# Performance work log

Measured on AMD Instinct MI355X. Metric: run time of the kernel, lower is better.

Reference implementation:

```python
import jax, jax.numpy as jnp
import numpy as np

B, S, D = 32, 512, 512      # batch, seq, feature
E, H, O, K = 8, 2048, 512, 2  # experts, expert hidden, expert out, top_k


def setup_inputs() -> dict:
    key = jax.random.key(0)
    ks = jax.random.split(key, 5)
    sc = lambda k, shape, scale: jax.random.normal(k, shape, jnp.float32) * scale
    return {
        "x": sc(ks[0], (B, S, D), 1.0),
        "attn_w": sc(ks[1], (D, 1), 0.05),
        "attn_b": jnp.zeros((1,), jnp.float32),
        "gate_w": sc(ks[2], (D, E), 0.05),
        "gate_b": jnp.zeros((E,), jnp.float32),
        "w1": sc(ks[3], (E, D, H), 0.02),
        "b1": jnp.zeros((E, H), jnp.float32),
        "w2": sc(ks[4], (E, H, O), 0.02),
        "b2": jnp.zeros((E, O), jnp.float32),
    }


def reference(x, attn_w, attn_b, gate_w, gate_b, w1, b1, w2, b2):
    # --- attention pooling over the sequence axis ---
    scores = x @ attn_w + attn_b                      # [B,S,1]
    aw = jax.nn.softmax(scores, axis=1)               # softmax over seq
    pooled = jnp.sum(x * aw, axis=1)                  # [B,D]

    # --- gating: softmax -> top-k mask -> renormalize ---
    gates = jax.nn.softmax(pooled @ gate_w + gate_b, axis=-1)  # [B,E]
    _, idx = jax.lax.top_k(gates, K)                  # [B,K]
    mask = jnp.sum(jax.nn.one_hot(idx, E, dtype=gates.dtype), axis=-2)  # [B,E]
    g = gates * mask
    g = g / (jnp.sum(g, axis=-1, keepdims=True) + 1e-9)        # [B,E]

    # --- dense all-experts compute (exact GELU, as keras Dense('gelu')) ---
    h = jax.nn.gelu(jnp.einsum('bsd,edh->ebsh', x, w1) + b1[:, None, None, :],
                    approximate=False)                 # [E,B,S,H]
    eo = jax.nn.gelu(jnp.einsum('ebsh,eho->ebso', h, w2) + b2[:, None, None, :],
                     approximate=False)                # [E,B,S,O]

    # --- weighted combine over experts ---
    return jnp.einsum('ebso,be->bso', eo, g)           # [B,S,O]
```

## Files before the change

kernel.cpp:

```cpp
#include <hip/hip_runtime.h>
#include <hip/hip_bf16.h>
#include <math.h>

#define B_  32
#define S_  512
#define D_  512
#define E_  8
#define H_  2048
#define O_  512

typedef __bf16 bf16x8 __attribute__((ext_vector_type(8)));
typedef float  f32x4  __attribute__((ext_vector_type(4)));

#define GL2LDS(src, dst) \
  __builtin_amdgcn_global_load_lds((const __attribute__((address_space(1))) void*)(src), \
                                   (__attribute__((address_space(3))) void*)(dst), 16, 0, 0)

__device__ __forceinline__ float gelu_fast(float v) {
  float w = v * fmaf(v * v, 0.0713548162f, 1.5957691216f);
  float e = __expf(-w);
  return v * __builtin_amdgcn_rcpf(1.0f + e);
}

__device__ __forceinline__ float gelu_exact(float v) {
  return 0.5f * v * (1.0f + erff(v * 0.70710678118654752f));
}

__global__ __launch_bounds__(256) void pool_gate_kernel(
    const float* __restrict__ x, const float* __restrict__ attn_w,
    const float* __restrict__ attn_b, const float* __restrict__ gate_w,
    const float* __restrict__ gate_b, int* __restrict__ gidx, float* __restrict__ gwt)
{
  __shared__ float sc[512];
  __shared__ float pooled[512];
  __shared__ float red[8];
  const int tid = threadIdx.x;
  const int b = blockIdx.x;
  const float* xb = x + (size_t)b * S_ * D_;
  const float ab = attn_b[0];

  for (int s = tid; s < S_; s += 256) {
    const float4* xr = (const float4*)(xb + (size_t)s * D_);
    const float4* wr = (const float4*)attn_w;
    float acc = 0.f;
    for (int i = 0; i < D_ / 4; ++i) {
      float4 xv = xr[i], wv = wr[i];
      acc += xv.x * wv.x + xv.y * wv.y + xv.z * wv.z + xv.w * wv.w;
    }
    sc[s] = acc + ab;
  }
  __syncthreads();

  float m = fmaxf(sc[tid], sc[tid + 256]);
  for (int off = 32; off; off >>= 1) m = fmaxf(m, __shfl_down(m, off));
  if ((tid & 63) == 0) red[tid >> 6] = m;
  __syncthreads();
  if (tid == 0) red[0] = fmaxf(fmaxf(red[0], red[1]), fmaxf(red[2], red[3]));
  __syncthreads();
  m = red[0];
  float e0 = expf(sc[tid] - m), e1 = expf(sc[tid + 256] - m);
  float ssum = e0 + e1;
  for (int off = 32; off; off >>= 1) ssum += __shfl_down(ssum, off);
  if ((tid & 63) == 0) red[4 + (tid >> 6)] = ssum;
  __syncthreads();
  if (tid == 0) red[4] = red[4] + red[5] + red[6] + red[7];
  __syncthreads();
  float inv = 1.f / red[4];
  sc[tid] = e0 * inv;
  sc[tid + 256] = e1 * inv;
  __syncthreads();

  float p0 = 0.f, p1 = 0.f;
  for (int s = 0; s < S_; ++s) {
    float awv = sc[s];
    p0 += awv * xb[(size_t)s * D_ + tid];
    p1 += awv * xb[(size_t)s * D_ + tid + 256];
  }
  pooled[tid] = p0;
  pooled[tid + 256] = p1;
  __syncthreads();

  if (tid < E_) {
    float z = gate_b[tid];
    for (int d = 0; d < D_; ++d) z += pooled[d] * gate_w[d * E_ + tid];
    red[tid] = z;
  }
  __syncthreads();
  if (tid == 0) {
    float zmax = red[0];
    for (int i = 1; i < E_; ++i) zmax = fmaxf(zmax, red[i]);
    float ge[E_]; float zs = 0.f;
    for (int i = 0; i < E_; ++i) { ge[i] = expf(red[i] - zmax); zs += ge[i]; }
    for (int i = 0; i < E_; ++i) ge[i] /= zs;
    int i0 = 0;
    for (int i = 1; i < E_; ++i) if (ge[i] > ge[i0]) i0 = i;
    int i1 = -1;
    for (int i = 0; i < E_; ++i) if (i != i0 && (i1 < 0 || ge[i] > ge[i1])) i1 = i;
    float denom = ge[i0] + ge[i1] + 1e-9f;
    gidx[b * 2 + 0] = i0; gidx[b * 2 + 1] = i1;
    gwt[b * 2 + 0] = ge[i0] / denom; gwt[b * 2 + 1] = ge[i1] / denom;
  }
}

__global__ void psort_kernel(const int* __restrict__ gidx, int* __restrict__ psort) {
  if (threadIdx.x == 0 && blockIdx.x == 0) {
    int cnt[E_];
    for (int e = 0; e < E_; ++e) cnt[e] = 0;
    for (int p = 0; p < 2 * B_; ++p) cnt[gidx[p]]++;
    int pos[E_]; int s = 0;
    for (int e = 0; e < E_; ++e) { pos[e] = s; s += cnt[e]; }
    for (int p = 0; p < 2 * B_; ++p) psort[pos[gidx[p]]++] = p;
  }
}

__global__ void cast_x_kernel(const float* __restrict__ in, ushort* __restrict__ outp, int n) {
  int i = blockIdx.x * blockDim.x + threadIdx.x;
  const int n4 = n >> 2;
  for (; i < n4; i += gridDim.x * blockDim.x) {
    float4 v = ((const float4*)in)[i];
    ushort4 o;
    o.x = __builtin_bit_cast(unsigned short, __float2bfloat16(v.x));
    o.y = __builtin_bit_cast(unsigned short, __float2bfloat16(v.y));
    o.z = __builtin_bit_cast(unsigned short, __float2bfloat16(v.z));
    o.w = __builtin_bit_cast(unsigned short, __float2bfloat16(v.w));
    ((ushort4*)outp)[i] = o;
  }
}

__global__ void transpose_cast_kernel(const float* __restrict__ in,
                                      __hip_bfloat16* __restrict__ outT, int R, int C)
{
  __shared__ float tile[32][33];
  const int z = blockIdx.z;
  const float* inz = in + (size_t)z * R * C;
  __hip_bfloat16* outz = outT + (size_t)z * R * C;
  const int c0 = blockIdx.x * 32, r0 = blockIdx.y * 32;
  const int tx = threadIdx.x, ty = threadIdx.y;
#pragma unroll
  for (int jj = 0; jj < 4; ++jj) {
    int r = r0 + ty + jj * 8;
    tile[ty + jj * 8][tx] = inz[(size_t)r * C + c0 + tx];
  }
  __syncthreads();
#pragma unroll
  for (int jj = 0; jj < 4; ++jj) {
    int c = c0 + ty + jj * 8;
    outz[(size_t)c * R + r0 + tx] = __float2bfloat16(tile[tx][ty + jj * 8]);
  }
}

__device__ __forceinline__ void gemm_core(const char* __restrict__ Wg, const char* __restrict__ Xg,
                                          const int ldw, const int ldx, const int NT,
                                          char* lds, f32x4 (&acc)[4][4])
{
  const int tid = threadIdx.x;
  const int l = tid & 63;
  const int w = tid >> 6;
  const int wh = w >> 1;
  const int ws = w & 1;
  const int lr = l & 15;
  const int kc16 = ((l >> 4) & 3) << 4;
  const int swz = (lr & 7) << 4;
  const int kA = kc16 ^ swz;
  const int kB = (64 + kc16) ^ swz;
  const int aoff = wh * 8192 + lr * 128;
  const int boff = 32768 + ws * 8192 + lr * 128;

  const int rw = tid >> 3;
  const int cs = ((tid & 7) << 4) ^ ((rw & 7) << 4);
  const int dst = tid * 16;
  const char* pW0 = Wg + (size_t)(rw      ) * ldw + cs;
  const char* pW1 = Wg + (size_t)(rw +  64) * ldw + cs;
  const char* pW2 = Wg + (size_t)(rw + 128) * ldw + cs;
  const char* pW3 = Wg + (size_t)(rw + 192) * ldw + cs;
  const char* pX0 = Xg + (size_t)(rw      ) * ldx + cs;
  const char* pX1 = Xg + (size_t)(rw +  64) * ldx + cs;

  {
    char* q0 = lds;
    GL2LDS(pW0, q0 + dst);          GL2LDS(pW1, q0 + 8192 + dst);
    GL2LDS(pW2, q0 + 16384 + dst);  GL2LDS(pW3, q0 + 24576 + dst);
    GL2LDS(pX0, q0 + 32768 + dst);  GL2LDS(pX1, q0 + 40960 + dst);
    char* q1 = lds + 49152;
    GL2LDS(pW0 + 128, q1 + dst);          GL2LDS(pW1 + 128, q1 + 8192 + dst);
    GL2LDS(pW2 + 128, q1 + 16384 + dst);  GL2LDS(pW3 + 128, q1 + 24576 + dst);
    GL2LDS(pX0 + 128, q1 + 32768 + dst);  GL2LDS(pX1 + 128, q1 + 40960 + dst);
    pW0 += 256; pW1 += 256; pW2 += 256; pW3 += 256; pX0 += 256; pX1 += 256;
  }

  for (int t = 0; t < NT; ++t) {
    char* cur = lds + (t % 3) * 49152;
    char* nb  = lds + ((t + 2) % 3) * 49152;
    const bool pre = (t + 2 < NT);

    if (pre) {
      GL2LDS(pW0, nb + dst);
      GL2LDS(pW1, nb + 8192 + dst);
      GL2LDS(pW2, nb + 16384 + dst);
    }
    if (pre)             asm volatile("s_waitcnt vmcnt(9)" ::: "memory");
    else if (t + 1 < NT) asm volatile("s_waitcnt vmcnt(6)" ::: "memory");
    else                 asm volatile("s_waitcnt vmcnt(0)" ::: "memory");
    __builtin_amdgcn_s_barrier();
    __builtin_amdgcn_sched_barrier(0);
    {
      bf16x8 af[4], bfv[4];
#pragma unroll
      for (int r = 0; r < 4; ++r) af[r]  = *(const bf16x8*)(cur + aoff + r * 2048 + kA);
#pragma unroll
      for (int n = 0; n < 4; ++n) bfv[n] = *(const bf16x8*)(cur + boff + n * 2048 + kA);
      __builtin_amdgcn_s_setprio(1);
#pragma unroll
      for (int r = 0; r < 4; ++r)
#pragma unroll
        for (int n = 0; n < 4; ++n)
          acc[r][n] = __builtin_amdgcn_mfma_f32_16x16x32_bf16(af[r], bfv[n], acc[r][n], 0, 0, 0);
      __builtin_amdgcn_s_setprio(0);
    }
    __builtin_amdgcn_sched_barrier(0);
    __builtin_amdgcn_s_barrier();

    if (pre) {
      GL2LDS(pW3, nb + 24576 + dst);
      GL2LDS(pX0, nb + 32768 + dst);
      GL2LDS(pX1, nb + 40960 + dst);
      pW0 += 128; pW1 += 128; pW2 += 128; pW3 += 128; pX0 += 128; pX1 += 128;
    }
    {
      bf16x8 af[4], bfv[4];
#pragma unroll
      for (int r = 0; r < 4; ++r) af[r]  = *(const bf16x8*)(cur + aoff + r * 2048 + kB);
#pragma unroll
      for (int n = 0; n < 4; ++n) bfv[n] = *(const bf16x8*)(cur + boff + n * 2048 + kB);
      __builtin_amdgcn_s_setprio(1);
#pragma unroll
      for (int r = 0; r < 4; ++r)
#pragma unroll
        for (int n = 0; n < 4; ++n)
          acc[r][n] = __builtin_amdgcn_mfma_f32_16x16x32_bf16(af[r], bfv[n], acc[r][n], 0, 0, 0);
      __builtin_amdgcn_s_setprio(0);
    }
    __builtin_amdgcn_sched_barrier(0);
    __builtin_amdgcn_s_barrier();
  }
}

__global__ __launch_bounds__(512, 2) void gemm1_kernel(
    const __hip_bfloat16* __restrict__ Xb, const __hip_bfloat16* __restrict__ W1T,
    const float* __restrict__ b1, __hip_bfloat16* __restrict__ Hbuf,
    const int* __restrict__ gidx, const int* __restrict__ psort)
{
  extern __shared__ char lds[];
  const int nblk = gridDim.x * gridDim.y;
  const int P = blockIdx.y * gridDim.x + blockIdx.x;
  const int L = (P & 7) * (nblk >> 3) + (P >> 3);
  const int pairL = L >> 5;
  const int tl = L & 31;
  const int p = psort[pairL];
  const int b = p >> 1;
  const int e = gidx[p];
  const int s0 = (tl >> 3) * 128;
  const int h0 = (tl & 7) * 256;
  const char* Wg = (const char*)(W1T + ((size_t)e * H_ + h0) * D_);
  const char* Xg = (const char*)(Xb + ((size_t)b * S_ + s0) * D_);
  f32x4 acc[4][4] = {};
  gemm_core(Wg, Xg, D_ * 2, D_ * 2, D_ / 64, lds, acc);

  const int tid = threadIdx.x, l = tid & 63, w = tid >> 6;
  const int wh = w >> 1, ws = w & 1, lr = l & 15, hi4 = ((l >> 4) & 3) << 2;
  const float* b1e = b1 + (size_t)e * H_ + h0;
  __hip_bfloat16* Hp = Hbuf + (size_t)p * S_ * H_;
#pragma unroll
  for (int r = 0; r < 4; ++r) {
    const int hl = wh * 64 + r * 16 + hi4;
    const float4 bias = *(const float4*)(b1e + hl);
#pragma unroll
    for (int n = 0; n < 4; ++n) {
      const int sl = s0 + ws * 64 + n * 16 + lr;
      ushort4 ov;
      ov.x = __builtin_bit_cast(unsigned short, __float2bfloat16(gelu_fast(acc[r][n][0] + bias.x)));
      ov.y = __builtin_bit_cast(unsigned short, __float2bfloat16(gelu_fast(acc[r][n][1] + bias.y)));
      ov.z = __builtin_bit_cast(unsigned short, __float2bfloat16(gelu_fast(acc[r][n][2] + bias.z)));
      ov.w = __builtin_bit_cast(unsigned short, __float2bfloat16(gelu_fast(acc[r][n][3] + bias.w)));
      *(ushort4*)(Hp + (size_t)sl * H_ + h0 + hl) = ov;
    }
  }
}

__global__ __launch_bounds__(512, 2) void gemm2_kernel(
    const __hip_bfloat16* __restrict__ Hbuf, const __hip_bfloat16* __restrict__ W2T,
    const float* __restrict__ b2, float* __restrict__ out,
    const int* __restrict__ gidx, const float* __restrict__ gwt)
{
  extern __shared__ char lds[];
  const int nblk = gridDim.x * gridDim.y;
  const int P = blockIdx.y * gridDim.x + blockIdx.x;
  const int L = (P & 7) * (nblk >> 3) + (P >> 3);
  const int b = L >> 3;
  const int tl = L & 7;
  const int s0 = (tl >> 1) * 128;
  const int o0 = (tl & 1) * 256;

  const int tid = threadIdx.x, l = tid & 63, w = tid >> 6;
  const int wh = w >> 1, ws = w & 1, lr = l & 15, hi4 = ((l >> 4) & 3) << 2;

  f32x4 fout[4][4] = {};
  for (int slot = 0; slot < 2; ++slot) {
    const int p = b * 2 + slot;
    const int e = gidx[p];
    const float gw = gwt[p];
    const char* Wg = (const char*)(W2T + ((size_t)e * O_ + o0) * H_);
    const char* Xg = (const char*)(Hbuf + ((size_t)p * S_ + s0) * H_);
    f32x4 acc[4][4] = {};
    gemm_core(Wg, Xg, H_ * 2, H_ * 2, H_ / 64, lds, acc);
    const float* b2e = b2 + (size_t)e * O_ + o0;
#pragma unroll
    for (int r = 0; r < 4; ++r) {
      const int ol = wh * 64 + r * 16 + hi4;
      const float4 bias = *(const float4*)(b2e + ol);
#pragma unroll
      for (int n = 0; n < 4; ++n) {
        fout[r][n][0] += gelu_fast(acc[r][n][0] + bias.x) * gw;
        fout[r][n][1] += gelu_fast(acc[r][n][1] + bias.y) * gw;
        fout[r][n][2] += gelu_fast(acc[r][n][2] + bias.z) * gw;
        fout[r][n][3] += gelu_fast(acc[r][n][3] + bias.w) * gw;
      }
    }
  }

#pragma unroll
  for (int r = 0; r < 4; ++r) {
    const int ol = wh * 64 + r * 16 + hi4;
#pragma unroll
    for (int n = 0; n < 4; ++n) {
      const int sl = s0 + ws * 64 + n * 16 + lr;
      *(float4*)(out + ((size_t)b * S_ + sl) * O_ + o0 + ol) =
          (float4){fout[r][n][0], fout[r][n][1], fout[r][n][2], fout[r][n][3]};
    }
  }
}

__global__ void sentinel_kernel(float* out, int n) {
  int i = blockIdx.x * blockDim.x + threadIdx.x;
  for (; i < n; i += gridDim.x * blockDim.x) out[i] = 1.0e6f;
}

extern "C" void kernel_launch(void* const* d_in, const int* in_sizes, int n_in,
                              void* d_out, int out_size, void* d_ws, size_t ws_size,
                              hipStream_t stream)
{
  const float* x      = (const float*)d_in[0];
  const float* attn_w = (const float*)d_in[1];
  const float* attn_b = (const float*)d_in[2];
  const float* gate_w = (const float*)d_in[3];
  const float* gate_b = (const float*)d_in[4];
  const float* w1     = (const float*)d_in[5];
  const float* b1     = (const float*)d_in[6];
  const float* w2     = (const float*)d_in[7];
  const float* b2     = (const float*)d_in[8];
  float* out = (float*)d_out;

  char* ws = (char*)d_ws;
  const size_t OFF_GIDX = 0;
  const size_t OFF_GWT  = 256;
  const size_t OFF_PSRT = 512;
  const size_t OFF_X    = 1024;
  const size_t SZ_X     = (size_t)B_ * S_ * D_ * 2;
  const size_t OFF_W1T  = OFF_X + SZ_X;
  const size_t SZ_W1T   = (size_t)E_ * H_ * D_ * 2;
  const size_t OFF_W2T  = OFF_W1T + SZ_W1T;
  const size_t SZ_W2T   = (size_t)E_ * O_ * H_ * 2;
  const size_t OFF_H    = OFF_W2T + SZ_W2T;
  const size_t PAIR_H   = (size_t)S_ * H_ * 2;

  if (OFF_H + 64 * PAIR_H > ws_size) {
    hipLaunchKernelGGL(sentinel_kernel, dim3(256), dim3(256), 0, stream, out, out_size);
    return;
  }

  int*   gidx  = (int*)(ws + OFF_GIDX);
  float* gwt   = (float*)(ws + OFF_GWT);
  int*   psort = (int*)(ws + OFF_PSRT);
  __hip_bfloat16* xb   = (__hip_bfloat16*)(ws + OFF_X);
  __hip_bfloat16* w1T  = (__hip_bfloat16*)(ws + OFF_W1T);
  __hip_bfloat16* w2T  = (__hip_bfloat16*)(ws + OFF_W2T);
  __hip_bfloat16* Hbuf = (__hip_bfloat16*)(ws + OFF_H);

  (void)hipFuncSetAttribute((const void*)gemm1_kernel, hipFuncAttributeMaxDynamicSharedMemorySize, 147456);
  (void)hipFuncSetAttribute((const void*)gemm2_kernel, hipFuncAttributeMaxDynamicSharedMemorySize, 147456);

  hipLaunchKernelGGL(pool_gate_kernel, dim3(B_), dim3(256), 0, stream,
                     x, attn_w, attn_b, gate_w, gate_b, gidx, gwt);
  hipLaunchKernelGGL(psort_kernel, dim3(1), dim3(64), 0, stream, gidx, psort);
  hipLaunchKernelGGL(cast_x_kernel, dim3(2048), dim3(256), 0, stream,
                     x, (ushort*)xb, B_ * S_ * D_);
  hipLaunchKernelGGL(transpose_cast_kernel, dim3(H_ / 32, D_ / 32, E_), dim3(32, 8), 0, stream,
                     w1, w1T, D_, H_);
  hipLaunchKernelGGL(transpose_cast_kernel, dim3(O_ / 32, H_ / 32, E_), dim3(32, 8), 0, stream,
                     w2, w2T, H_, O_);

  hipLaunchKernelGGL(gemm1_kernel, dim3(32, 64), dim3(512), 147456, stream,
                     xb, w1T, b1, Hbuf, gidx, psort);
  hipLaunchKernelGGL(gemm2_kernel, dim3(8, 32), dim3(512), 147456, stream,
                     Hbuf, w2T, b2, out, gidx, gwt);
}
```

Measured before the change: 290.0 us.

## Parallelize attention pooling and run persistent continuous-K pipelines in both expert GEMMs

The single 32-block pool/gate kernel is split into four stages: a fused bf16 cast plus score dot-product, a per-batch softmax, a pooling kernel spread over a 4x32 grid, and a combined gate/top-k/sort kernel. The attention bias is dropped because softmax over the sequence is shift-invariant. GEMM1 now launches 256 blocks, and each block streams all 8 H tiles through one continuous triple-buffered pipeline, writing its epilogue every 8 steps. GEMM2 chains both expert slots into a single 64-step pipeline, which removes the pipeline drain and refill between slots. The cost is fewer blocks per GPU, which lowers occupancy and load balancing, and the score, weight and pooled scratch buffers now live in the H buffer region.

After: 269.3 us. 7.2% less time.

```diff
diff --git a/kernel.cpp b/kernel.cpp
--- a/kernel.cpp
+++ b/kernel.cpp
@@ -22,108 +22,123 @@
   return v * __builtin_amdgcn_rcpf(1.0f + e);
 }
 
-__device__ __forceinline__ float gelu_exact(float v) {
-  return 0.5f * v * (1.0f + erff(v * 0.70710678118654752f));
-}
-
-__global__ __launch_bounds__(256) void pool_gate_kernel(
+__global__ __launch_bounds__(256) void cast_score_kernel(
     const float* __restrict__ x, const float* __restrict__ attn_w,
-    const float* __restrict__ attn_b, const float* __restrict__ gate_w,
-    const float* __restrict__ gate_b, int* __restrict__ gidx, float* __restrict__ gwt)
-{
-  __shared__ float sc[512];
-  __shared__ float pooled[512];
-  __shared__ float red[8];
-  const int tid = threadIdx.x;
-  const int b = blockIdx.x;
-  const float* xb = x + (size_t)b * S_ * D_;
-  const float ab = attn_b[0];
-
-  for (int s = tid; s < S_; s += 256) {
-    const float4* xr = (const float4*)(xb + (size_t)s * D_);
-    const float4* wr = (const float4*)attn_w;
-    float acc = 0.f;
-    for (int i = 0; i < D_ / 4; ++i) {
-      float4 xv = xr[i], wv = wr[i];
-      acc += xv.x * wv.x + xv.y * wv.y + xv.z * wv.z + xv.w * wv.w;
-    }
-    sc[s] = acc + ab;
-  }
-  __syncthreads();
-
-  float m = fmaxf(sc[tid], sc[tid + 256]);
-  for (int off = 32; off; off >>= 1) m = fmaxf(m, __shfl_down(m, off));
-  if ((tid & 63) == 0) red[tid >> 6] = m;
-  __syncthreads();
-  if (tid == 0) red[0] = fmaxf(fmaxf(red[0], red[1]), fmaxf(red[2], red[3]));
-  __syncthreads();
-  m = red[0];
-  float e0 = expf(sc[tid] - m), e1 = expf(sc[tid + 256] - m);
-  float ssum = e0 + e1;
-  for (int off = 32; off; off >>= 1) ssum += __shfl_down(ssum, off);
-  if ((tid & 63) == 0) red[4 + (tid >> 6)] = ssum;
-  __syncthreads();
-  if (tid == 0) red[4] = red[4] + red[5] + red[6] + red[7];
-  __syncthreads();
-  float inv = 1.f / red[4];
-  sc[tid] = e0 * inv;
-  sc[tid + 256] = e1 * inv;
-  __syncthreads();
-
-  float p0 = 0.f, p1 = 0.f;
-  for (int s = 0; s < S_; ++s) {
-    float awv = sc[s];
-    p0 += awv * xb[(size_t)s * D_ + tid];
-    p1 += awv * xb[(size_t)s * D_ + tid + 256];
-  }
-  pooled[tid] = p0;
-  pooled[tid + 256] = p1;
-  __syncthreads();
-
-  if (tid < E_) {
-    float z = gate_b[tid];
-    for (int d = 0; d < D_; ++d) z += pooled[d] * gate_w[d * E_ + tid];
-    red[tid] = z;
-  }
-  __syncthreads();
-  if (tid == 0) {
-    float zmax = red[0];
-    for (int i = 1; i < E_; ++i) zmax = fmaxf(zmax, red[i]);
-    float ge[E_]; float zs = 0.f;
-    for (int i = 0; i < E_; ++i) { ge[i] = expf(red[i] - zmax); zs += ge[i]; }
-    for (int i = 0; i < E_; ++i) ge[i] /= zs;
-    int i0 = 0;
-    for (int i = 1; i < E_; ++i) if (ge[i] > ge[i0]) i0 = i;
-    int i1 = -1;
-    for (int i = 0; i < E_; ++i) if (i != i0 && (i1 < 0 || ge[i] > ge[i1])) i1 = i;
-    float denom = ge[i0] + ge[i1] + 1e-9f;
-    gidx[b * 2 + 0] = i0; gidx[b * 2 + 1] = i1;
-    gwt[b * 2 + 0] = ge[i0] / denom; gwt[b * 2 + 1] = ge[i1] / denom;
-  }
-}
-
-__global__ void psort_kernel(const int* __restrict__ gidx, int* __restrict__ psort) {
-  if (threadIdx.x == 0 && blockIdx.x == 0) {
-    int cnt[E_];
-    for (int e = 0; e < E_; ++e) cnt[e] = 0;
-    for (int p = 0; p < 2 * B_; ++p) cnt[gidx[p]]++;
-    int pos[E_]; int s = 0;
-    for (int e = 0; e < E_; ++e) { pos[e] = s; s += cnt[e]; }
-    for (int p = 0; p < 2 * B_; ++p) psort[pos[gidx[p]]++] = p;
-  }
-}
-
-__global__ void cast_x_kernel(const float* __restrict__ in, ushort* __restrict__ outp, int n) {
-  int i = blockIdx.x * blockDim.x + threadIdx.x;
-  const int n4 = n >> 2;
-  for (; i < n4; i += gridDim.x * blockDim.x) {
-    float4 v = ((const float4*)in)[i];
+    ushort* __restrict__ xb, float* __restrict__ scores)
+{
+  const int t = threadIdx.x;
+  const int r = t >> 5;
+  const int cg = t & 31;
+  const int row = blockIdx.x * 8 + r;
+  const float* src  = x + (size_t)row * D_ + cg * 16;
+  const float* wsrc = attn_w + cg * 16;
+  ushort* dstp = xb + (size_t)row * D_ + cg * 16;
+  float acc = 0.f;
+#pragma unroll
+  for (int k = 0; k < 4; ++k) {
+    float4 v  = *(const float4*)(src + k * 4);
+    float4 wv = *(const float4*)(wsrc + k * 4);
+    acc += v.x * wv.x + v.y * wv.y + v.z * wv.z + v.w * wv.w;
     ushort4 o;
     o.x = __builtin_bit_cast(unsigned short, __float2bfloat16(v.x));
     o.y = __builtin_bit_cast(unsigned short, __float2bfloat16(v.y));
     o.z = __builtin_bit_cast(unsigned short, __float2bfloat16(v.z));
     o.w = __builtin_bit_cast(unsigned short, __float2bfloat16(v.w));
-    ((ushort4*)outp)[i] = o;
+    *(ushort4*)(dstp + k * 4) = o;
+  }
+#pragma unroll
+  for (int off = 16; off; off >>= 1) acc += __shfl_xor(acc, off);
+  if (cg == 0) scores[row] = acc;
+}
+
+__global__ __launch_bounds__(512) void softmax_aw_kernel(
+    const float* __restrict__ scores, float* __restrict__ aw)
+{
+  __shared__ float red[8];
+  __shared__ float mm, ss;
+  const int t = threadIdx.x, b = blockIdx.x;
+  float v = scores[b * S_ + t];
+  float m = v;
+#pragma unroll
+  for (int off = 32; off; off >>= 1) m = fmaxf(m, __shfl_xor(m, off));
+  if ((t & 63) == 0) red[t >> 6] = m;
+  __syncthreads();
+  if (t == 0) {
+    float a = red[0];
+    for (int i = 1; i < 8; ++i) a = fmaxf(a, red[i]);
+    mm = a;
+  }
+  __syncthreads();
+  float e = expf(v - mm);
+  float s = e;
+#pragma unroll
+  for (int off = 32; off; off >>= 1) s += __shfl_xor(s, off);
+  if ((t & 63) == 0) red[t >> 6] = s;
+  __syncthreads();
+  if (t == 0) {
+    float a = 0.f;
+    for (int i = 0; i < 8; ++i) a += red[i];
+    ss = 1.f / a;
+  }
+  __syncthreads();
+  aw[b * S_ + t] = e * ss;
+}
+
+__global__ __launch_bounds__(512) void pool_kernel(
+    const float* __restrict__ x, const float* __restrict__ aw, float* __restrict__ pooled)
+{
+  __shared__ float sm[4][128];
+  const int t = threadIdx.x;
+  const int dl = t & 127;
+  const int sh = t >> 7;
+  const int b = blockIdx.y;
+  const int d = blockIdx.x * 128 + dl;
+  const float* xp  = x + (size_t)b * S_ * D_ + d;
+  const float* awb = aw + b * S_;
+  float acc = 0.f;
+#pragma unroll 4
+  for (int s = sh; s < S_; s += 4)
+    acc = fmaf(awb[s], xp[(size_t)s * D_], acc);
+  if (sh) sm[sh][dl] = acc;
+  __syncthreads();
+  if (sh == 0) pooled[b * D_ + d] = acc + sm[1][dl] + sm[2][dl] + sm[3][dl];
+}
+
+__global__ __launch_bounds__(256) void gate_psort_kernel(
+    const float* __restrict__ pooled, const float* __restrict__ gate_w,
+    const float* __restrict__ gate_b, int* __restrict__ gidx, float* __restrict__ gwt,
+    int* __restrict__ psort)
+{
+  __shared__ float gl[32][8];
+  const int t = threadIdx.x;
+  const int b = t >> 3, ee = t & 7;
+  float z = gate_b[ee];
+  const float* pb = pooled + b * D_;
+  for (int d = 0; d < D_; ++d) z = fmaf(pb[d], gate_w[d * E_ + ee], z);
+  gl[b][ee] = z;
+  __syncthreads();
+  if (t < 32) {
+    float ge[8];
+    float zmax = gl[t][0];
+    for (int i = 1; i < 8; ++i) zmax = fmaxf(zmax, gl[t][i]);
+    float zs = 0.f;
+    for (int i = 0; i < 8; ++i) { ge[i] = expf(gl[t][i] - zmax); zs += ge[i]; }
+    for (int i = 0; i < 8; ++i) ge[i] /= zs;
+    int i0 = 0;
+    for (int i = 1; i < 8; ++i) if (ge[i] > ge[i0]) i0 = i;
+    int i1 = -1;
+    for (int i = 0; i < 8; ++i) if (i != i0 && (i1 < 0 || ge[i] > ge[i1])) i1 = i;
+    float denom = ge[i0] + ge[i1] + 1e-9f;
+    gidx[t * 2 + 0] = i0; gidx[t * 2 + 1] = i1;
+    gwt[t * 2 + 0] = ge[i0] / denom; gwt[t * 2 + 1] = ge[i1] / denom;
+  }
+  __syncthreads();
+  if (t == 0) {
+    int cnt[E_] = {}, pos[E_];
+    for (int p = 0; p < 2 * B_; ++p) cnt[gidx[p]]++;
+    int s = 0;
+    for (int e2 = 0; e2 < E_; ++e2) { pos[e2] = s; s += cnt[e2]; }
+    for (int p = 0; p < 2 * B_; ++p) psort[pos[gidx[p]]++] = p;
   }
 }
 
@@ -149,142 +164,121 @@
   }
 }
 
-__device__ __forceinline__ void gemm_core(const char* __restrict__ Wg, const char* __restrict__ Xg,
-                                          const int ldw, const int ldx, const int NT,
-                                          char* lds, f32x4 (&acc)[4][4])
-{
+__device__ __forceinline__ void phase_mfma(const char* cur, int aoff, int boff, int koff,
+                                           f32x4 (&acc)[4][4])
+{
+  bf16x8 af[4], bfv[4];
+#pragma unroll
+  for (int r = 0; r < 4; ++r) af[r]  = *(const bf16x8*)(cur + aoff + r * 2048 + koff);
+#pragma unroll
+  for (int n = 0; n < 4; ++n) bfv[n] = *(const bf16x8*)(cur + boff + n * 2048 + koff);
+  __builtin_amdgcn_s_setprio(1);
+#pragma unroll
+  for (int r = 0; r < 4; ++r)
+#pragma unroll
+    for (int n = 0; n < 4; ++n)
+      acc[r][n] = __builtin_amdgcn_mfma_f32_16x16x32_bf16(af[r], bfv[n], acc[r][n], 0, 0, 0);
+  __builtin_amdgcn_s_setprio(0);
+}
+
+__global__ __launch_bounds__(512, 2) void gemm1_kernel(
+    const __hip_bfloat16* __restrict__ Xb, const __hip_bfloat16* __restrict__ W1T,
+    const float* __restrict__ b1, __hip_bfloat16* __restrict__ Hbuf,
+    const int* __restrict__ gidx, const int* __restrict__ psort)
+{
+  extern __shared__ char lds[];
   const int tid = threadIdx.x;
-  const int l = tid & 63;
-  const int w = tid >> 6;
-  const int wh = w >> 1;
-  const int ws = w & 1;
+  const int P = blockIdx.x;
+  const int n_ = (P & 7) * 32 + (P >> 3);
+  const int p = psort[n_ >> 2];
+  const int b = p >> 1;
+  const int e = gidx[p];
+  const int s0 = (n_ & 3) * 128;
+
+  const char* Wbase = (const char*)W1T + (size_t)e * H_ * D_ * 2;
+  const char* Xgb   = (const char*)Xb + ((size_t)b * S_ + s0) * D_ * 2;
+
+  const int rw = tid >> 3;
+  const int laneoff = rw * (D_ * 2) + ((((tid & 7) << 4)) ^ ((rw & 7) << 4));
+  const int dst = tid * 16;
+
+  const int l = tid & 63, w = tid >> 6;
+  const int wh = w >> 1, ws_ = w & 1;
   const int lr = l & 15;
   const int kc16 = ((l >> 4) & 3) << 4;
   const int swz = (lr & 7) << 4;
   const int kA = kc16 ^ swz;
   const int kB = (64 + kc16) ^ swz;
   const int aoff = wh * 8192 + lr * 128;
-  const int boff = 32768 + ws * 8192 + lr * 128;
-
-  const int rw = tid >> 3;
-  const int cs = ((tid & 7) << 4) ^ ((rw & 7) << 4);
-  const int dst = tid * 16;
-  const char* pW0 = Wg + (size_t)(rw      ) * ldw + cs;
-  const char* pW1 = Wg + (size_t)(rw +  64) * ldw + cs;
-  const char* pW2 = Wg + (size_t)(rw + 128) * ldw + cs;
-  const char* pW3 = Wg + (size_t)(rw + 192) * ldw + cs;
-  const char* pX0 = Xg + (size_t)(rw      ) * ldx + cs;
-  const char* pX1 = Xg + (size_t)(rw +  64) * ldx + cs;
-
-  {
-    char* q0 = lds;
-    GL2LDS(pW0, q0 + dst);          GL2LDS(pW1, q0 + 8192 + dst);
-    GL2LDS(pW2, q0 + 16384 + dst);  GL2LDS(pW3, q0 + 24576 + dst);
-    GL2LDS(pX0, q0 + 32768 + dst);  GL2LDS(pX1, q0 + 40960 + dst);
-    char* q1 = lds + 49152;
-    GL2LDS(pW0 + 128, q1 + dst);          GL2LDS(pW1 + 128, q1 + 8192 + dst);
-    GL2LDS(pW2 + 128, q1 + 16384 + dst);  GL2LDS(pW3 + 128, q1 + 24576 + dst);
-    GL2LDS(pX0 + 128, q1 + 32768 + dst);  GL2LDS(pX1 + 128, q1 + 40960 + dst);
-    pW0 += 256; pW1 += 256; pW2 += 256; pW3 += 256; pX0 += 256; pX1 += 256;
-  }
-
-  for (int t = 0; t < NT; ++t) {
-    char* cur = lds + (t % 3) * 49152;
-    char* nb  = lds + ((t + 2) % 3) * 49152;
-    const bool pre = (t + 2 < NT);
-
-    if (pre) {
-      GL2LDS(pW0, nb + dst);
-      GL2LDS(pW1, nb + 8192 + dst);
-      GL2LDS(pW2, nb + 16384 + dst);
+  const int boff = 32768 + ws_ * 8192 + lr * 128;
+  const int hi4 = ((l >> 4) & 3) << 2;
+
+#define G1_STAGE_A(us, nb) { \
+    const char* wsrc = Wbase + (((us) >> 3) << 18) + (((us) & 7) << 7) + laneoff; \
+    GL2LDS(wsrc,          (nb) + dst); \
+    GL2LDS(wsrc + 65536,  (nb) + 8192 + dst); \
+    GL2LDS(wsrc + 131072, (nb) + 16384 + dst); }
+#define G1_STAGE_B(us, nb) { \
+    const char* wsrc = Wbase + (((us) >> 3) << 18) + (((us) & 7) << 7) + laneoff; \
+    GL2LDS(wsrc + 196608, (nb) + 24576 + dst); \
+    const char* xsrc = Xgb + (((us) & 7) << 7) + laneoff; \
+    GL2LDS(xsrc,          (nb) + 32768 + dst); \
+    GL2LDS(xsrc + 65536,  (nb) + 40960 + dst); }
+
+  f32x4 acc[4][4] = {};
+  __hip_bfloat16* Hp = Hbuf + (size_t)p * S_ * H_;
+  const float* b1e0 = b1 + (size_t)e * H_;
+
+  G1_STAGE_A(0, lds); G1_STAGE_B(0, lds);
+  G1_STAGE_A(1, lds + 49152); G1_STAGE_B(1, lds + 49152);
+
+  int cu = 0;
+#pragma unroll 1
+  for (int u = 0; u < 64; ++u) {
+    char* cur = lds + cu * 49152;
+    char* nb  = lds + ((cu >= 1) ? (cu - 1) : (cu + 2)) * 49152;
+    if (u < 62) {
+      G1_STAGE_A(u + 2, nb);
+      asm volatile("s_waitcnt vmcnt(9)" ::: "memory");
+    } else if (u == 62) {
+      asm volatile("s_waitcnt vmcnt(6)" ::: "memory");
+    } else {
+      asm volatile("s_waitcnt vmcnt(0)" ::: "memory");
     }
-    if (pre)             asm volatile("s_waitcnt vmcnt(9)" ::: "memory");
-    else if (t + 1 < NT) asm volatile("s_waitcnt vmcnt(6)" ::: "memory");
-    else                 asm volatile("s_waitcnt vmcnt(0)" ::: "memory");
-    __builtin_amdgcn_s_barrier();
-    __builtin_amdgcn_sched_barrier(0);
-    {
-      bf16x8 af[4], bfv[4];
-#pragma unroll
-      for (int r = 0; r < 4; ++r) af[r]  = *(const bf16x8*)(cur + aoff + r * 2048 + kA);
-#pragma unroll
-      for (int n = 0; n < 4; ++n) bfv[n] = *(const bf16x8*)(cur + boff + n * 2048 + kA);
-      __builtin_amdgcn_s_setprio(1);
-#pragma unroll
-      for (int r = 0; r < 4; ++r)
-#pragma unroll
-        for (int n = 0; n < 4; ++n)
-          acc[r][n] = __builtin_amdgcn_mfma_f32_16x16x32_bf16(af[r], bfv[n], acc[r][n], 0, 0, 0);
-      __builtin_amdgcn_s_setprio(0);
+    __builtin_amdgcn_s_barrier();
+    __builtin_amdgcn_sched_barrier(0);
+    phase_mfma(cur, aoff, boff, kA, acc);
+    __builtin_amdgcn_sched_barrier(0);
+    __builtin_amdgcn_s_barrier();
+    if (u < 62) G1_STAGE_B(u + 2, nb);
+    phase_mfma(cur, aoff, boff, kB, acc);
+    __builtin_amdgcn_sched_barrier(0);
+    __builtin_amdgcn_s_barrier();
+
+    if ((u & 7) == 7) {
+      const int h0 = (u >> 3) << 8;
+      const float* b1e = b1e0 + h0;
+#pragma unroll
+      for (int r = 0; r < 4; ++r) {
+        const int hl = wh * 64 + r * 16 + hi4;
+        const float4 bias = *(const float4*)(b1e + hl);
+#pragma unroll
+        for (int n = 0; n < 4; ++n) {
+          const int sl = s0 + ws_ * 64 + n * 16 + lr;
+          ushort4 ov;
+          ov.x = __builtin_bit_cast(unsigned short, __float2bfloat16(gelu_fast(acc[r][n][0] + bias.x)));
+          ov.y = __builtin_bit_cast(unsigned short, __float2bfloat16(gelu_fast(acc[r][n][1] + bias.y)));
+          ov.z = __builtin_bit_cast(unsigned short, __float2bfloat16(gelu_fast(acc[r][n][2] + bias.z)));
+          ov.w = __builtin_bit_cast(unsigned short, __float2bfloat16(gelu_fast(acc[r][n][3] + bias.w)));
+          *(ushort4*)(Hp + (size_t)sl * H_ + h0 + hl) = ov;
+          acc[r][n] = (f32x4){0.f, 0.f, 0.f, 0.f};
+        }
+      }
     }
-    __builtin_amdgcn_sched_barrier(0);
-    __builtin_amdgcn_s_barrier();
-
-    if (pre) {
-      GL2LDS(pW3, nb + 24576 + dst);
-      GL2LDS(pX0, nb + 32768 + dst);
-      GL2LDS(pX1, nb + 40960 + dst);
-      pW0 += 128; pW1 += 128; pW2 += 128; pW3 += 128; pX0 += 128; pX1 += 128;
-    }
-    {
-      bf16x8 af[4], bfv[4];
-#pragma unroll
-      for (int r = 0; r < 4; ++r) af[r]  = *(const bf16x8*)(cur + aoff + r * 2048 + kB);
-#pragma unroll
-      for (int n = 0; n < 4; ++n) bfv[n] = *(const bf16x8*)(cur + boff + n * 2048 + kB);
-      __builtin_amdgcn_s_setprio(1);
-#pragma unroll
-      for (int r = 0; r < 4; ++r)
-#pragma unroll
-        for (int n = 0; n < 4; ++n)
-          acc[r][n] = __builtin_amdgcn_mfma_f32_16x16x32_bf16(af[r], bfv[n], acc[r][n], 0, 0, 0);
-      __builtin_amdgcn_s_setprio(0);
-    }
-    __builtin_amdgcn_sched_barrier(0);
-    __builtin_amdgcn_s_barrier();
-  }
-}
-
-__global__ __launch_bounds__(512, 2) void gemm1_kernel(
-    const __hip_bfloat16* __restrict__ Xb, const __hip_bfloat16* __restrict__ W1T,
-    const float* __restrict__ b1, __hip_bfloat16* __restrict__ Hbuf,
-    const int* __restrict__ gidx, const int* __restrict__ psort)
-{
-  extern __shared__ char lds[];
-  const int nblk = gridDim.x * gridDim.y;
-  const int P = blockIdx.y * gridDim.x + blockIdx.x;
-  const int L = (P & 7) * (nblk >> 3) + (P >> 3);
-  const int pairL = L >> 5;
-  const int tl = L & 31;
-  const int p = psort[pairL];
-  const int b = p >> 1;
-  const int e = gidx[p];
-  const int s0 = (tl >> 3) * 128;
-  const int h0 = (tl & 7) * 256;
-  const char* Wg = (const char*)(W1T + ((size_t)e * H_ + h0) * D_);
-  const char* Xg = (const char*)(Xb + ((size_t)b * S_ + s0) * D_);
-  f32x4 acc[4][4] = {};
-  gemm_core(Wg, Xg, D_ * 2, D_ * 2, D_ / 64, lds, acc);
-
-  const int tid = threadIdx.x, l = tid & 63, w = tid >> 6;
-  const int wh = w >> 1, ws = w & 1, lr = l & 15, hi4 = ((l >> 4) & 3) << 2;
-  const float* b1e = b1 + (size_t)e * H_ + h0;
-  __hip_bfloat16* Hp = Hbuf + (size_t)p * S_ * H_;
-#pragma unroll
-  for (int r = 0; r < 4; ++r) {
-    const int hl = wh * 64 + r * 16 + hi4;
-    const float4 bias = *(const float4*)(b1e + hl);
-#pragma unroll
-    for (int n = 0; n < 4; ++n) {
-      const int sl = s0 + ws * 64 + n * 16 + lr;
-      ushort4 ov;
-      ov.x = __builtin_bit_cast(unsigned short, __float2bfloat16(gelu_fast(acc[r][n][0] + bias.x)));
-      ov.y = __builtin_bit_cast(unsigned short, __float2bfloat16(gelu_fast(acc[r][n][1] + bias.y)));
-      ov.z = __builtin_bit_cast(unsigned short, __float2bfloat16(gelu_fast(acc[r][n][2] + bias.z)));
-      ov.w = __builtin_bit_cast(unsigned short, __float2bfloat16(gelu_fast(acc[r][n][3] + bias.w)));
-      *(ushort4*)(Hp + (size_t)sl * H_ + h0 + hl) = ov;
-    }
-  }
+    cu = (cu == 2) ? 0 : cu + 1;
+  }
+#undef G1_STAGE_A
+#undef G1_STAGE_B
 }
 
 __global__ __launch_bounds__(512, 2) void gemm2_kernel(
@@ -293,47 +287,107 @@
     const int* __restrict__ gidx, const float* __restrict__ gwt)
 {
   extern __shared__ char lds[];
-  const int nblk = gridDim.x * gridDim.y;
-  const int P = blockIdx.y * gridDim.x + blockIdx.x;
-  const int L = (P & 7) * (nblk >> 3) + (P >> 3);
-  const int b = L >> 3;
-  const int tl = L & 7;
+  const int tid = threadIdx.x;
+  const int P = blockIdx.x;
+  const int n_ = (P & 7) * 32 + (P >> 3);
+  const int b = n_ >> 3;
+  const int tl = n_ & 7;
   const int s0 = (tl >> 1) * 128;
   const int o0 = (tl & 1) * 256;
 
-  const int tid = threadIdx.x, l = tid & 63, w = tid >> 6;
-  const int wh = w >> 1, ws = w & 1, lr = l & 15, hi4 = ((l >> 4) & 3) << 2;
-
+  const int e0 = gidx[2 * b], e1 = gidx[2 * b + 1];
+  const float gw0 = gwt[2 * b], gw1 = gwt[2 * b + 1];
+
+  const int rw = tid >> 3;
+  const int laneoff = rw * (H_ * 2) + ((((tid & 7) << 4)) ^ ((rw & 7) << 4));
+  const int dst = tid * 16;
+
+  const char* W0p = (const char*)W2T + ((size_t)e0 * O_ + o0) * H_ * 2;
+  const char* W1p = (const char*)W2T + ((size_t)e1 * O_ + o0) * H_ * 2;
+  const char* X0p = (const char*)Hbuf + ((size_t)(2 * b)     * S_ + s0) * H_ * 2;
+  const char* X1p = (const char*)Hbuf + ((size_t)(2 * b + 1) * S_ + s0) * H_ * 2;
+
+  const int l = tid & 63, w = tid >> 6;
+  const int wh = w >> 1, ws_ = w & 1;
+  const int lr = l & 15;
+  const int kc16 = ((l >> 4) & 3) << 4;
+  const int swz = (lr & 7) << 4;
+  const int kA = kc16 ^ swz;
+  const int kB = (64 + kc16) ^ swz;
+  const int aoff = wh * 8192 + lr * 128;
+  const int boff = 32768 + ws_ * 8192 + lr * 128;
+  const int hi4 = ((l >> 4) & 3) << 2;
+
+#define G2_STAGE_A(us, nb) { \
+    const char* wsrc = (((us) & 32) ? W1p : W0p) + (((us) & 31) << 7) + laneoff; \
+    GL2LDS(wsrc,          (nb) + dst); \
+    GL2LDS(wsrc + 262144, (nb) + 8192 + dst); \
+    GL2LDS(wsrc + 524288, (nb) + 16384 + dst); }
+#define G2_STAGE_B(us, nb) { \
+    const char* wsrc = (((us) & 32) ? W1p : W0p) + (((us) & 31) << 7) + laneoff; \
+    GL2LDS(wsrc + 786432, (nb) + 24576 + dst); \
+    const char* xsrc = (((us) & 32) ? X1p : X0p) + (((us) & 31) << 7) + laneoff; \
+    GL2LDS(xsrc,          (nb) + 32768 + dst); \
+    GL2LDS(xsrc + 262144, (nb) + 40960 + dst); }
+
+  f32x4 acc[4][4] = {};
   f32x4 fout[4][4] = {};
-  for (int slot = 0; slot < 2; ++slot) {
-    const int p = b * 2 + slot;
-    const int e = gidx[p];
-    const float gw = gwt[p];
-    const char* Wg = (const char*)(W2T + ((size_t)e * O_ + o0) * H_);
-    const char* Xg = (const char*)(Hbuf + ((size_t)p * S_ + s0) * H_);
-    f32x4 acc[4][4] = {};
-    gemm_core(Wg, Xg, H_ * 2, H_ * 2, H_ / 64, lds, acc);
-    const float* b2e = b2 + (size_t)e * O_ + o0;
-#pragma unroll
-    for (int r = 0; r < 4; ++r) {
-      const int ol = wh * 64 + r * 16 + hi4;
-      const float4 bias = *(const float4*)(b2e + ol);
-#pragma unroll
-      for (int n = 0; n < 4; ++n) {
-        fout[r][n][0] += gelu_fast(acc[r][n][0] + bias.x) * gw;
-        fout[r][n][1] += gelu_fast(acc[r][n][1] + bias.y) * gw;
-        fout[r][n][2] += gelu_fast(acc[r][n][2] + bias.z) * gw;
-        fout[r][n][3] += gelu_fast(acc[r][n][3] + bias.w) * gw;
+
+  G2_STAGE_A(0, lds); G2_STAGE_B(0, lds);
+  G2_STAGE_A(1, lds + 49152); G2_STAGE_B(1, lds + 49152);
+
+  int cu = 0;
+#pragma unroll 1
+  for (int u = 0; u < 64; ++u) {
+    char* cur = lds + cu * 49152;
+    char* nb  = lds + ((cu >= 1) ? (cu - 1) : (cu + 2)) * 49152;
+    if (u < 62) {
+      G2_STAGE_A(u + 2, nb);
+      asm volatile("s_waitcnt vmcnt(9)" ::: "memory");
+    } else if (u == 62) {
+      asm volatile("s_waitcnt vmcnt(6)" ::: "memory");
+    } else {
+      asm volatile("s_waitcnt vmcnt(0)" ::: "memory");
+    }
+    __builtin_amdgcn_s_barrier();
+    __builtin_amdgcn_sched_barrier(0);
+    phase_mfma(cur, aoff, boff, kA, acc);
+    __builtin_amdgcn_sched_barrier(0);
+    __builtin_amdgcn_s_barrier();
+    if (u < 62) G2_STAGE_B(u + 2, nb);
+    phase_mfma(cur, aoff, boff, kB, acc);
+    __builtin_amdgcn_sched_barrier(0);
+    __builtin_amdgcn_s_barrier();
+
+    if ((u & 31) == 31) {
+      const int slot = u >> 5;
+      const float gw = slot ? gw1 : gw0;
+      const float* b2e = b2 + (size_t)(slot ? e1 : e0) * O_ + o0;
+#pragma unroll
+      for (int r = 0; r < 4; ++r) {
+        const int ol = wh * 64 + r * 16 + hi4;
+        const float4 bias = *(const float4*)(b2e + ol);
+#pragma unroll
+        for (int n = 0; n < 4; ++n) {
+          fout[r][n][0] += gelu_fast(acc[r][n][0] + bias.x) * gw;
+          fout[r][n][1] += gelu_fast(acc[r][n][1] + bias.y) * gw;
+          fout[r][n][2] += gelu_fast(acc[r][n][2] + bias.z) * gw;
+          fout[r][n][3] += gelu_fast(acc[r][n][3] + bias.w) * gw;
+          acc[r][n] = (f32x4){0.f, 0.f, 0.f, 0.f};
+        }
       }
     }
-  }
+    cu = (cu == 2) ? 0 : cu + 1;
+  }
+#undef G2_STAGE_A
+#undef G2_STAGE_B
 
 #pragma unroll
   for (int r = 0; r < 4; ++r) {
     const int ol = wh * 64 + r * 16 + hi4;
 #pragma unroll
     for (int n = 0; n < 4; ++n) {
-      const int sl = s0 + ws * 64 + n * 16 + lr;
+      const int sl = s0 + ws_ * 64 + n * 16 + lr;
       *(float4*)(out + ((size_t)b * S_ + sl) * O_ + o0 + ol) =
           (float4){fout[r][n][0], fout[r][n][1], fout[r][n][2], fout[r][n][3]};
     }
@@ -351,7 +405,6 @@
 {
   const float* x      = (const float*)d_in[0];
   const float* attn_w = (const float*)d_in[1];
-  const float* attn_b = (const float*)d_in[2];
   const float* gate_w = (const float*)d_in[3];
   const float* gate_b = (const float*)d_in[4];
   const float* w1     = (const float*)d_in[5];
@@ -385,22 +438,26 @@
   __hip_bfloat16* w1T  = (__hip_bfloat16*)(ws + OFF_W1T);
   __hip_bfloat16* w2T  = (__hip_bfloat16*)(ws + OFF_W2T);
   __hip_bfloat16* Hbuf = (__hip_bfloat16*)(ws + OFF_H);
+  float* scores = (float*)(ws + OFF_H);
+  float* aw     = (float*)(ws + OFF_H + 65536);
+  float* pooled = (float*)(ws + OFF_H + 131072);
 
   (void)hipFuncSetAttribute((const void*)gemm1_kernel, hipFuncAttributeMaxDynamicSharedMemorySize, 147456);
   (void)hipFuncSetAttribute((const void*)gemm2_kernel, hipFuncAttributeMaxDynamicSharedMemorySize, 147456);
 
-  hipLaunchKernelGGL(pool_gate_kernel, dim3(B_), dim3(256), 0, stream,
-                     x, attn_w, attn_b, gate_w, gate_b, gidx, gwt);
-  hipLaunchKernelGGL(psort_kernel, dim3(1), dim3(64), 0, stream, gidx, psort);
-  hipLaunchKernelGGL(cast_x_kernel, dim3(2048), dim3(256), 0, stream,
-                     x, (ushort*)xb, B_ * S_ * D_);
+  hipLaunchKernelGGL(cast_score_kernel, dim3(B_ * S_ / 8), dim3(256), 0, stream,
+                     x, attn_w, (ushort*)xb, scores);
+  hipLaunchKernelGGL(softmax_aw_kernel, dim3(B_), dim3(512), 0, stream, scores, aw);
+  hipLaunchKernelGGL(pool_kernel, dim3(4, B_), dim3(512), 0, stream, x, aw, pooled);
+  hipLaunchKernelGGL(gate_psort_kernel, dim3(1), dim3(256), 0, stream,
+                     pooled, gate_w, gate_b, gidx, gwt, psort);
   hipLaunchKernelGGL(transpose_cast_kernel, dim3(H_ / 32, D_ / 32, E_), dim3(32, 8), 0, stream,
                      w1, w1T, D_, H_);
   hipLaunchKernelGGL(transpose_cast_kernel, dim3(O_ / 32, H_ / 32, E_), dim3(32, 8), 0, stream,
                      w2, w2T, H_, O_);
 
-  hipLaunchKernelGGL(gemm1_kernel, dim3(32, 64), dim3(512), 147456, stream,
+  hipLaunchKernelGGL(gemm1_kernel, dim3(256), dim3(512), 147456, stream,
                      xb, w1T, b1, Hbuf, gidx, psort);
-  hipLaunchKernelGGL(gemm2_kernel, dim3(8, 32), dim3(512), 147456, stream,
+  hipLaunchKernelGGL(gemm2_kernel, dim3(256), dim3(512), 147456, stream,
                      Hbuf, w2T, b2, out, gidx, gwt);
 }
```
